# Optimization experiments

Hardware: AMD Instinct MI355X
Metric: run time of the kernel (lower is better)

Reference implementation:

```python
import jax, jax.numpy as jnp
import numpy as np

B, IN, H = 8192, 1024, 1024


def setup_inputs() -> dict:
    key = jax.random.key(0)
    ks = jax.random.split(key, 20)
    std = 1.0 / np.sqrt(H)
    u = lambda k, shape: jax.random.uniform(k, shape, jnp.float32, -std, std)
    inp = {
        "x": jax.random.normal(ks[0], (B, IN), jnp.float32),
        "hx": jax.random.normal(ks[1], (B, H), jnp.float32),
        "cx": jax.random.normal(ks[2], (B, H), jnp.float32),
        "task_id": 0,
        # x2h weights [H, IN] (torch Linear layout) and biases [H]
        "wxi": u(ks[3], (H, IN)), "bxi": u(ks[4], (H,)),
        "wxf": u(ks[5], (H, IN)), "bxf": u(ks[6], (H,)),
        "wxc": u(ks[7], (H, IN)), "bxc": u(ks[8], (H,)),
        "wxo": u(ks[9], (H, IN)), "bxo": u(ks[10], (H,)),
        # h2h weights [H, H] and biases [H]
        "whi": u(ks[11], (H, H)), "bhi": u(ks[12], (H,)),
        "whf": u(ks[13], (H, H)), "bhf": u(ks[14], (H,)),
        "whc": u(ks[15], (H, H)), "bhc": u(ks[16], (H,)),
        "who": u(ks[17], (H, H)), "bho": u(ks[18], (H,)),
    }
    return inp


def reference(x, hx, cx, task_id,
              wxi, bxi, wxf, bxf, wxc, bxc, wxo, bxo,
              whi, bhi, whf, bhf, whc, bhc, who, bho):
    # x = x.view(-1, x.size(1)) is identity for 2D input
    # gate pre-activations: Linear(x) + Linear(hx)  (torch: x @ W.T + b)
    ingate = x @ wxi.T + bxi + hx @ whi.T + bhi
    forgetgate = x @ wxf.T + bxf + hx @ whf.T + bhf
    cellgate = x @ wxc.T + bxc + hx @ whc.T + bhc
    outgate = x @ wxo.T + bxo + hx @ who.T + bho

    i = jax.nn.sigmoid(ingate)
    f = jax.nn.sigmoid(forgetgate)
    g = jnp.tanh(cellgate)
    o = jax.nn.sigmoid(outgate)

    cy = cx * f + i * g
    hy = o * jnp.tanh(cy)
    return hy, cy
```

## Files before the change

kernel.cpp:

```cpp
#include <hip/hip_runtime.h>
#include <hip/hip_bf16.h>

#define B_DIM  8192
#define IN_DIM 1024
#define H_DIM  1024
#define K_DIM  2048

typedef __attribute__((ext_vector_type(8))) short bf16x8;
typedef __attribute__((ext_vector_type(4))) float f32x4;

__device__ __forceinline__ void mfma_16x16x32_bf16(f32x4& d, const bf16x8& a, const bf16x8& b) {
  asm("v_mfma_f32_16x16x32_bf16 %0, %1, %2, %0" : "+v"(d) : "v"(a), "v"(b));
}

__device__ __forceinline__ void gload16(const void* g, void* l) {
  __builtin_amdgcn_global_load_lds(
      (const __attribute__((address_space(1))) void*)g,
      (__attribute__((address_space(3))) void*)l,
      16, 0, 0);
}

__device__ __forceinline__ float fast_sigmoid(float x) {
  return 1.0f / (1.0f + __expf(-x));
}
__device__ __forceinline__ float fast_tanh(float x) {
  float e = __expf(2.0f * x);
  return 1.0f - 2.0f / (e + 1.0f);
}

__global__ __launch_bounds__(256) void pack_a_kernel(
    const float* __restrict__ x, const float* __restrict__ hx,
    __hip_bfloat16* __restrict__ A) {
  const int idx = blockIdx.x * 256 + threadIdx.x;
  const int r  = idx >> 8;
  const int kk = (idx & 255) << 3;
  const float* src = (kk < IN_DIM) ? (x + (size_t)r * IN_DIM + kk)
                                   : (hx + (size_t)r * H_DIM + (kk - IN_DIM));
  const float4 v0 = ((const float4*)src)[0];
  const float4 v1 = ((const float4*)src)[1];
  __hip_bfloat16 t[8];
  t[0] = __float2bfloat16(v0.x); t[1] = __float2bfloat16(v0.y);
  t[2] = __float2bfloat16(v0.z); t[3] = __float2bfloat16(v0.w);
  t[4] = __float2bfloat16(v1.x); t[5] = __float2bfloat16(v1.y);
  t[6] = __float2bfloat16(v1.z); t[7] = __float2bfloat16(v1.w);
  *(uint4*)(A + ((size_t)idx << 3)) = *(const uint4*)t;
}

__global__ __launch_bounds__(256) void pack_w_kernel(
    const float* __restrict__ wxi, const float* __restrict__ wxf,
    const float* __restrict__ wxc, const float* __restrict__ wxo,
    const float* __restrict__ whi, const float* __restrict__ whf,
    const float* __restrict__ whc, const float* __restrict__ who,
    __hip_bfloat16* __restrict__ W) {
  const int idx = blockIdx.x * 256 + threadIdx.x;
  const int row = idx >> 8;
  const int kk  = (idx & 255) << 3;
  const int g = row >> 10, n = row & 1023;
  const float* src;
  if (kk < IN_DIM) {
    const float* p = (g == 0) ? wxi : (g == 1) ? wxf : (g == 2) ? wxc : wxo;
    src = p + (size_t)n * IN_DIM + kk;
  } else {
    const float* p = (g == 0) ? whi : (g == 1) ? whf : (g == 2) ? whc : who;
    src = p + (size_t)n * H_DIM + (kk - IN_DIM);
  }
  const float4 v0 = ((const float4*)src)[0];
  const float4 v1 = ((const float4*)src)[1];
  __hip_bfloat16 t[8];
  t[0] = __float2bfloat16(v0.x); t[1] = __float2bfloat16(v0.y);
  t[2] = __float2bfloat16(v0.z); t[3] = __float2bfloat16(v0.w);
  t[4] = __float2bfloat16(v1.x); t[5] = __float2bfloat16(v1.y);
  t[6] = __float2bfloat16(v1.z); t[7] = __float2bfloat16(v1.w);
  *(uint4*)(W + ((size_t)idx << 3)) = *(const uint4*)t;
}

__global__ __launch_bounds__(256, 2) void lstm_gemm_kernel(
    const __hip_bfloat16* __restrict__ A,
    const __hip_bfloat16* __restrict__ W,
    const float* __restrict__ cx,
    const float* __restrict__ bxi, const float* __restrict__ bhi,
    const float* __restrict__ bxf, const float* __restrict__ bhf,
    const float* __restrict__ bxc, const float* __restrict__ bhc,
    const float* __restrict__ bxo, const float* __restrict__ bho,
    float* __restrict__ hy, float* __restrict__ cy) {

  __shared__ __align__(16) __hip_bfloat16 sA[128][64];
  __shared__ __align__(16) __hip_bfloat16 sW[4][64][64];

  const int tid  = threadIdx.x;
  const int w    = tid >> 6;
  const int lane = tid & 63;
  const int wm = w >> 1, wn = w & 1;
  const int lq = lane >> 4, lr16 = lane & 15;

  const int row0 = blockIdx.x * 128;
  const int col0 = blockIdx.y * 64;

  const int sr  = lane >> 3;
  const int sc  = lane & 7;
  const int scs = sc ^ sr;

  f32x4 acc[4][4][2];
#pragma unroll
  for (int g = 0; g < 4; ++g)
#pragma unroll
    for (int m = 0; m < 4; ++m)
#pragma unroll
      for (int nf = 0; nf < 2; ++nf)
        acc[g][m][nf] = (f32x4){0.f, 0.f, 0.f, 0.f};

  for (int kt = 0; kt < K_DIM / 64; ++kt) {
    const int k0 = kt * 64;
#pragma unroll
    for (int it = 0; it < 4; ++it) {
      const int stripe = it * 4 + w;
      const int fr = stripe * 8 + sr;
      const __hip_bfloat16* src = A + (size_t)(row0 + fr) * K_DIM + k0 + scs * 8;
      gload16(src, (char*)(&sA[0][0]) + stripe * 1024);
    }
#pragma unroll
    for (int it = 0; it < 8; ++it) {
      const int stripe = it * 4 + w;
      const int fr = stripe * 8 + sr;
      const int g = fr >> 6, n = fr & 63;
      const __hip_bfloat16* src =
          W + ((size_t)(g << 10) + col0 + n) * K_DIM + k0 + scs * 8;
      gload16(src, (char*)(&sW[0][0][0]) + stripe * 1024);
    }
    __syncthreads();

#pragma unroll
    for (int ks = 0; ks < 2; ++ks) {
      bf16x8 af[4];
#pragma unroll
      for (int m = 0; m < 4; ++m) {
        const int row = wm * 64 + m * 16 + lr16;
        const int ch  = (ks * 4 + lq) ^ (row & 7);
        af[m] = *(const bf16x8*)&sA[row][ch * 8];
      }
#pragma unroll
      for (int g = 0; g < 4; ++g) {
        bf16x8 bfv[2];
#pragma unroll
        for (int nf = 0; nf < 2; ++nf) {
          const int n  = wn * 32 + nf * 16 + lr16;
          const int ch = (ks * 4 + lq) ^ (n & 7);
          bfv[nf] = *(const bf16x8*)&sW[g][n][ch * 8];
        }
#pragma unroll
        for (int m = 0; m < 4; ++m)
#pragma unroll
          for (int nf = 0; nf < 2; ++nf)
            mfma_16x16x32_bf16(acc[g][m][nf], af[m], bfv[nf]);
      }
    }
    __syncthreads();
  }

#pragma unroll
  for (int nf = 0; nf < 2; ++nf) {
    const int h = col0 + wn * 32 + nf * 16 + lr16;
    const float bi = bxi[h] + bhi[h];
    const float bf = bxf[h] + bhf[h];
    const float bc = bxc[h] + bhc[h];
    const float bo = bxo[h] + bho[h];
#pragma unroll
    for (int m = 0; m < 4; ++m) {
#pragma unroll
      for (int j = 0; j < 4; ++j) {
        const int r = row0 + wm * 64 + m * 16 + lq * 4 + j;
        const size_t o = (size_t)r * H_DIM + h;
        const float ig = fast_sigmoid(acc[0][m][nf][j] + bi);
        const float fg = fast_sigmoid(acc[1][m][nf][j] + bf);
        const float gg = fast_tanh   (acc[2][m][nf][j] + bc);
        const float og = fast_sigmoid(acc[3][m][nf][j] + bo);
        const float c  = cx[o] * fg + ig * gg;
        cy[o] = c;
        hy[o] = og * fast_tanh(c);
      }
    }
  }
}

extern "C" void kernel_launch(void* const* d_in, const int* in_sizes, int n_in,
                              void* d_out, int out_size, void* d_ws, size_t ws_size,
                              hipStream_t stream) {
  const float* x   = (const float*)d_in[0];
  const float* hx  = (const float*)d_in[1];
  const float* cx  = (const float*)d_in[2];
  const float* wxi = (const float*)d_in[4];  const float* bxi = (const float*)d_in[5];
  const float* wxf = (const float*)d_in[6];  const float* bxf = (const float*)d_in[7];
  const float* wxc = (const float*)d_in[8];  const float* bxc = (const float*)d_in[9];
  const float* wxo = (const float*)d_in[10]; const float* bxo = (const float*)d_in[11];
  const float* whi = (const float*)d_in[12]; const float* bhi = (const float*)d_in[13];
  const float* whf = (const float*)d_in[14]; const float* bhf = (const float*)d_in[15];
  const float* whc = (const float*)d_in[16]; const float* bhc = (const float*)d_in[17];
  const float* who = (const float*)d_in[18]; const float* bho = (const float*)d_in[19];

  __hip_bfloat16* Abf = (__hip_bfloat16*)d_ws;
  __hip_bfloat16* Wbf = (__hip_bfloat16*)((char*)d_ws + (size_t)B_DIM * K_DIM * 2);

  float* hy  = (float*)d_out;
  float* cyo = (float*)d_out + (size_t)B_DIM * H_DIM;

  pack_a_kernel<<<(B_DIM * K_DIM / 8) / 256, 256, 0, stream>>>(x, hx, Abf);
  pack_w_kernel<<<(4 * H_DIM * K_DIM / 8) / 256, 256, 0, stream>>>(
      wxi, wxf, wxc, wxo, whi, whf, whc, who, Wbf);

  dim3 grid(B_DIM / 128, H_DIM / 64);
  lstm_gemm_kernel<<<grid, 256, 0, stream>>>(
      Abf, Wbf, cx, bxi, bhi, bxf, bhf, bxc, bhc, bxo, bho, hy, cyo);
}
```

Before: 155.3 us.

## Double-buffer LDS tiles with 256x64 blocks, 8 waves, and phased MFMA/load overlap

Restructures the fused LSTM GEMM so each 512-thread block covers a 256-row by 64-column tile (all four gates), with double-buffered LDS for the A and W tiles. Global-to-LDS loads for the next K step are issued in chunks between MFMA phases, and partial vmcnt waits replace the full syncthreads pairs, so memory latency overlaps compute. It also adds a grouped block-index swizzle for L2 locality and raises MFMA priority with s_setprio. The cost is doubled LDS use (about 128 KB per block) and heavier register pressure, which may limit occupancy.

```diff
diff --git a/kernel.cpp b/kernel.cpp
--- a/kernel.cpp
+++ b/kernel.cpp
@@ -5,6 +5,7 @@
 #define IN_DIM 1024
 #define H_DIM  1024
 #define K_DIM  2048
+#define NT     (K_DIM / 64)
 
 typedef __attribute__((ext_vector_type(8))) short bf16x8;
 typedef __attribute__((ext_vector_type(4))) float f32x4;
@@ -74,7 +75,31 @@
   *(uint4*)(W + ((size_t)idx << 3)) = *(const uint4*)t;
 }
 
-__global__ __launch_bounds__(256, 2) void lstm_gemm_kernel(
+struct PhaseRegs {
+  f32x4 (&acc)[4][8];
+  const bf16x8 (&bfr)[4][2];
+};
+
+template<int MB>
+__device__ __forceinline__ void do_phase(
+    const __hip_bfloat16 (*sAp)[64], f32x4 (&acc)[4][8],
+    const bf16x8 (&bfr)[4][2], int arow, int chk0, int chk1) {
+  bf16x8 a00 = *(const bf16x8*)&sAp[arow + MB * 16][chk0];
+  bf16x8 a01 = *(const bf16x8*)&sAp[arow + MB * 16][chk1];
+  bf16x8 a10 = *(const bf16x8*)&sAp[arow + (MB + 1) * 16][chk0];
+  bf16x8 a11 = *(const bf16x8*)&sAp[arow + (MB + 1) * 16][chk1];
+  __builtin_amdgcn_s_setprio(1);
+#pragma unroll
+  for (int g = 0; g < 4; ++g) {
+    mfma_16x16x32_bf16(acc[g][MB],     a00, bfr[g][0]);
+    mfma_16x16x32_bf16(acc[g][MB],     a01, bfr[g][1]);
+    mfma_16x16x32_bf16(acc[g][MB + 1], a10, bfr[g][0]);
+    mfma_16x16x32_bf16(acc[g][MB + 1], a11, bfr[g][1]);
+  }
+  __builtin_amdgcn_s_setprio(0);
+}
+
+__global__ __launch_bounds__(512, 2) void lstm_gemm_kernel(
     const __hip_bfloat16* __restrict__ A,
     const __hip_bfloat16* __restrict__ W,
     const float* __restrict__ cx,
@@ -84,102 +109,109 @@
     const float* __restrict__ bxo, const float* __restrict__ bho,
     float* __restrict__ hy, float* __restrict__ cy) {
 
-  __shared__ __align__(16) __hip_bfloat16 sA[128][64];
-  __shared__ __align__(16) __hip_bfloat16 sW[4][64][64];
+  __shared__ __align__(16) __hip_bfloat16 sA[2][256][64];
+  __shared__ __align__(16) __hip_bfloat16 sW[2][4][64][64];
 
   const int tid  = threadIdx.x;
   const int w    = tid >> 6;
   const int lane = tid & 63;
-  const int wm = w >> 1, wn = w & 1;
+  const int wm = w >> 2, wn = w & 3;
   const int lq = lane >> 4, lr16 = lane & 15;
 
-  const int row0 = blockIdx.x * 128;
-  const int col0 = blockIdx.y * 64;
-
-  const int sr  = lane >> 3;
-  const int sc  = lane & 7;
-  const int scs = sc ^ sr;
-
-  f32x4 acc[4][4][2];
+  const int bid = blockIdx.x;
+  const int swz = (bid & 7) * 64 + (bid >> 3);
+  const int row0 = (swz >> 4) * 256;
+  const int col0 = (swz & 15) * 64;
+
+  const int srow = tid >> 3;
+  const int scs  = (tid & 7) ^ (srow & 7);
+  const __hip_bfloat16* Asrc = A + (size_t)(row0 + srow) * K_DIM + scs * 8;
+  const __hip_bfloat16* Wsrc = W + (size_t)(col0 + srow) * K_DIM + scs * 8;
+  const size_t Wg = (size_t)H_DIM * K_DIM;
+
+  const int chk0 = ((lq)     ^ (lr16 & 7)) * 8;
+  const int chk1 = ((4 + lq) ^ (lr16 & 7)) * 8;
+  const int arow = wm * 128 + lr16;
+  const int wrow = wn * 16 + lr16;
+
+  f32x4 acc[4][8];
 #pragma unroll
   for (int g = 0; g < 4; ++g)
 #pragma unroll
-    for (int m = 0; m < 4; ++m)
-#pragma unroll
-      for (int nf = 0; nf < 2; ++nf)
-        acc[g][m][nf] = (f32x4){0.f, 0.f, 0.f, 0.f};
-
-  for (int kt = 0; kt < K_DIM / 64; ++kt) {
-    const int k0 = kt * 64;
-#pragma unroll
-    for (int it = 0; it < 4; ++it) {
-      const int stripe = it * 4 + w;
-      const int fr = stripe * 8 + sr;
-      const __hip_bfloat16* src = A + (size_t)(row0 + fr) * K_DIM + k0 + scs * 8;
-      gload16(src, (char*)(&sA[0][0]) + stripe * 1024);
+    for (int m = 0; m < 8; ++m)
+      acc[g][m] = (f32x4){0.f, 0.f, 0.f, 0.f};
+
+#define ISSUE_W2(P, KT, G0)                                                    \
+  {                                                                            \
+    const size_t kof = (size_t)(KT) * 64;                                      \
+    gload16(Wsrc + (size_t)(G0) * Wg + kof,                                    \
+            (char*)&sW[P][G0][0][0] + tid * 16);                               \
+    gload16(Wsrc + (size_t)((G0) + 1) * Wg + kof,                              \
+            (char*)&sW[P][(G0) + 1][0][0] + tid * 16);                         \
+  }
+#define ISSUE_A2(P, KT, R0, R1)                                                \
+  {                                                                            \
+    const size_t kof = (size_t)(KT) * 64;                                      \
+    gload16(Asrc + (size_t)(R0) * K_DIM + kof,                                 \
+            (char*)&sA[P][R0][0] + tid * 16);                                  \
+    gload16(Asrc + (size_t)(R1) * K_DIM + kof,                                 \
+            (char*)&sA[P][R1][0] + tid * 16);                                  \
+  }
+
+  ISSUE_W2(0, 0, 0);
+  ISSUE_W2(0, 0, 2);
+  ISSUE_A2(0, 0, 0, 128);
+  ISSUE_A2(0, 0, 64, 192);
+
+  for (int t = 0; t < NT; ++t) {
+    const int p  = t & 1;
+    const int q  = p ^ 1;
+    const int tn = (t + 1 < NT) ? t + 1 : NT - 1;
+    const __hip_bfloat16(*sAp)[64] = sA[p];
+
+    ISSUE_W2(q, tn, 0);
+    asm volatile("s_waitcnt vmcnt(4)\n\ts_barrier" ::: "memory");
+    bf16x8 bfr[4][2];
+#pragma unroll
+    for (int g = 0; g < 4; ++g) {
+      bfr[g][0] = *(const bf16x8*)&sW[p][g][wrow][chk0];
+      bfr[g][1] = *(const bf16x8*)&sW[p][g][wrow][chk1];
     }
-#pragma unroll
-    for (int it = 0; it < 8; ++it) {
-      const int stripe = it * 4 + w;
-      const int fr = stripe * 8 + sr;
-      const int g = fr >> 6, n = fr & 63;
-      const __hip_bfloat16* src =
-          W + ((size_t)(g << 10) + col0 + n) * K_DIM + k0 + scs * 8;
-      gload16(src, (char*)(&sW[0][0][0]) + stripe * 1024);
+    do_phase<0>(sAp, acc, bfr, arow, chk0, chk1);
+
+    ISSUE_W2(q, tn, 2);
+    do_phase<2>(sAp, acc, bfr, arow, chk0, chk1);
+
+    ISSUE_A2(q, tn, 0, 128);
+    asm volatile("s_waitcnt vmcnt(6)\n\ts_barrier" ::: "memory");
+    do_phase<4>(sAp, acc, bfr, arow, chk0, chk1);
+
+    ISSUE_A2(q, tn, 64, 192);
+    do_phase<6>(sAp, acc, bfr, arow, chk0, chk1);
+  }
+
+  const int h = col0 + wrow;
+  const float bi = bxi[h] + bhi[h];
+  const float bf = bxf[h] + bhf[h];
+  const float bc = bxc[h] + bhc[h];
+  const float bo = bxo[h] + bho[h];
+#pragma unroll
+  for (int m = 0; m < 8; ++m) {
+#pragma unroll
+    for (int j = 0; j < 4; ++j) {
+      const int r = row0 + wm * 128 + m * 16 + lq * 4 + j;
+      const size_t o = (size_t)r * H_DIM + h;
+      const float ig = fast_sigmoid(acc[0][m][j] + bi);
+      const float fg = fast_sigmoid(acc[1][m][j] + bf);
+      const float gg = fast_tanh   (acc[2][m][j] + bc);
+      const float og = fast_sigmoid(acc[3][m][j] + bo);
+      const float c  = cx[o] * fg + ig * gg;
+      cy[o] = c;
+      hy[o] = og * fast_tanh(c);
     }
-    __syncthreads();
-
-#pragma unroll
-    for (int ks = 0; ks < 2; ++ks) {
-      bf16x8 af[4];
-#pragma unroll
-      for (int m = 0; m < 4; ++m) {
-        const int row = wm * 64 + m * 16 + lr16;
-        const int ch  = (ks * 4 + lq) ^ (row & 7);
-        af[m] = *(const bf16x8*)&sA[row][ch * 8];
-      }
-#pragma unroll
-      for (int g = 0; g < 4; ++g) {
-        bf16x8 bfv[2];
-#pragma unroll
-        for (int nf = 0; nf < 2; ++nf) {
-          const int n  = wn * 32 + nf * 16 + lr16;
-          const int ch = (ks * 4 + lq) ^ (n & 7);
-          bfv[nf] = *(const bf16x8*)&sW[g][n][ch * 8];
-        }
-#pragma unroll
-        for (int m = 0; m < 4; ++m)
-#pragma unroll
-          for (int nf = 0; nf < 2; ++nf)
-            mfma_16x16x32_bf16(acc[g][m][nf], af[m], bfv[nf]);
-      }
-    }
-    __syncthreads();
-  }
-
-#pragma unroll
-  for (int nf = 0; nf < 2; ++nf) {
-    const int h = col0 + wn * 32 + nf * 16 + lr16;
-    const float bi = bxi[h] + bhi[h];
-    const float bf = bxf[h] + bhf[h];
-    const float bc = bxc[h] + bhc[h];
-    const float bo = bxo[h] + bho[h];
-#pragma unroll
-    for (int m = 0; m < 4; ++m) {
-#pragma unroll
-      for (int j = 0; j < 4; ++j) {
-        const int r = row0 + wm * 64 + m * 16 + lq * 4 + j;
-        const size_t o = (size_t)r * H_DIM + h;
-        const float ig = fast_sigmoid(acc[0][m][nf][j] + bi);
-        const float fg = fast_sigmoid(acc[1][m][nf][j] + bf);
-        const float gg = fast_tanh   (acc[2][m][nf][j] + bc);
-        const float og = fast_sigmoid(acc[3][m][nf][j] + bo);
-        const float c  = cx[o] * fg + ig * gg;
-        cy[o] = c;
-        hy[o] = og * fast_tanh(c);
-      }
-    }
-  }
+  }
+#undef ISSUE_W2
+#undef ISSUE_A2
 }
 
 extern "C" void kernel_launch(void* const* d_in, const int* in_sizes, int n_in,
@@ -207,7 +239,6 @@
   pack_w_kernel<<<(4 * H_DIM * K_DIM / 8) / 256, 256, 0, stream>>>(
       wxi, wxf, wxc, wxo, whi, whf, whc, who, Wbf);
 
-  dim3 grid(B_DIM / 128, H_DIM / 64);
-  lstm_gemm_kernel<<<grid, 256, 0, stream>>>(
+  lstm_gemm_kernel<<<dim3(512), 512, 0, stream>>>(
       Abf, Wbf, cx, bxi, bhi, bxf, bhf, bxc, bhc, bxo, bho, hy, cyo);
 }
```

Measured after the change: 176.2 us. 13.5% more time.

## Double-buffer LDS with BK=32 prefetch pipeline and swizzled block order

Applied to the files above, without the earlier changes.

The GEMM loop is restructured into a two-stage LDS ping-pong with a K-tile of 32: the next tile's global-to-LDS loads are issued before computing on the current buffer, gated by a partial vmcnt wait plus barrier. The XOR swizzle is dropped in favour of a plain 64-byte row layout, and MFMA sections are wrapped in s_setprio. The grid becomes 1D with a remapped block-to-tile order so neighbouring blocks share weight columns for L2 reuse. The goal is to hide global load latency behind MFMA work. The trade-off is possible LDS bank conflicts from the unswizzled layout and twice as many barriers per unit of K.

```diff
diff --git a/kernel.cpp b/kernel.cpp
--- a/kernel.cpp
+++ b/kernel.cpp
@@ -5,6 +5,8 @@
 #define IN_DIM 1024
 #define H_DIM  1024
 #define K_DIM  2048
+#define BK     32
+#define NT     (K_DIM / BK)
 
 typedef __attribute__((ext_vector_type(8))) short bf16x8;
 typedef __attribute__((ext_vector_type(4))) float f32x4;
@@ -84,8 +86,7 @@
     const float* __restrict__ bxo, const float* __restrict__ bho,
     float* __restrict__ hy, float* __restrict__ cy) {
 
-  __shared__ __align__(16) __hip_bfloat16 sA[128][64];
-  __shared__ __align__(16) __hip_bfloat16 sW[4][64][64];
+  __shared__ __align__(16) char lds[2][24 * 1024];
 
   const int tid  = threadIdx.x;
   const int w    = tid >> 6;
@@ -93,12 +94,37 @@
   const int wm = w >> 1, wn = w & 1;
   const int lq = lane >> 4, lr16 = lane & 15;
 
-  const int row0 = blockIdx.x * 128;
-  const int col0 = blockIdx.y * 64;
-
-  const int sr  = lane >> 3;
-  const int sc  = lane & 7;
-  const int scs = sc ^ sr;
+  const int bid = blockIdx.x;
+  const int row_tile = ((bid & 7) << 3) | ((bid >> 3) & 7);
+  const int col_tile = bid >> 6;
+  const int row0 = row_tile * 128;
+  const int col0 = col_tile * 64;
+
+  const int srow = lane >> 2;
+  const int schk = lane & 3;
+
+  const __hip_bfloat16* gsrc[6];
+  int ldsoff[6];
+#pragma unroll
+  for (int s = 0; s < 6; ++s) {
+    const int seg = w * 6 + s;
+    if (seg < 8) {
+      gsrc[s] = A + (size_t)(row0 + seg * 16 + srow) * K_DIM + schk * 8;
+    } else {
+      const int flat = (seg - 8) * 16 + srow;
+      const int g = flat >> 6, n = flat & 63;
+      gsrc[s] = W + (size_t)((g << 10) + col0 + n) * K_DIM + schk * 8;
+    }
+    ldsoff[s] = seg * 1024;
+  }
+
+#define STAGE(Q, KT)                                                          \
+  {                                                                           \
+    const int koff = (KT) * BK;                                               \
+    _Pragma("unroll")                                                         \
+    for (int s = 0; s < 6; ++s)                                               \
+      gload16(gsrc[s] + koff, &lds[Q][ldsoff[s]]);                            \
+  }
 
   f32x4 acc[4][4][2];
 #pragma unroll
@@ -109,69 +135,59 @@
       for (int nf = 0; nf < 2; ++nf)
         acc[g][m][nf] = (f32x4){0.f, 0.f, 0.f, 0.f};
 
-  for (int kt = 0; kt < K_DIM / 64; ++kt) {
-    const int k0 = kt * 64;
-#pragma unroll
-    for (int it = 0; it < 4; ++it) {
-      const int stripe = it * 4 + w;
-      const int fr = stripe * 8 + sr;
-      const __hip_bfloat16* src = A + (size_t)(row0 + fr) * K_DIM + k0 + scs * 8;
-      gload16(src, (char*)(&sA[0][0]) + stripe * 1024);
-    }
-#pragma unroll
-    for (int it = 0; it < 8; ++it) {
-      const int stripe = it * 4 + w;
-      const int fr = stripe * 8 + sr;
-      const int g = fr >> 6, n = fr & 63;
-      const __hip_bfloat16* src =
-          W + ((size_t)(g << 10) + col0 + n) * K_DIM + k0 + scs * 8;
-      gload16(src, (char*)(&sW[0][0][0]) + stripe * 1024);
-    }
-    __syncthreads();
-
-#pragma unroll
-    for (int ks = 0; ks < 2; ++ks) {
-      bf16x8 af[4];
+  const int aoff = (wm * 64 + lr16) * 64 + lq * 16;
+  const int woff = 8192 + (wn * 32 + lr16) * 64 + lq * 16;
+
+  STAGE(0, 0);
+
+  for (int t = 0; t < NT; ++t) {
+    const int p = t & 1, q = p ^ 1;
+    const int tn = (t + 1 < NT) ? t + 1 : NT - 1;
+
+    STAGE(q, tn);
+    asm volatile("s_waitcnt vmcnt(6)\n\ts_barrier" ::: "memory");
+
+    const char* base = lds[p];
+    bf16x8 af[4];
+#pragma unroll
+    for (int m = 0; m < 4; ++m)
+      af[m] = *(const bf16x8*)(base + aoff + m * (16 * 64));
+
+    __builtin_amdgcn_s_setprio(1);
+#pragma unroll
+    for (int g = 0; g < 4; ++g) {
+      const char* wb = base + woff + g * (64 * 64);
+      const bf16x8 b0 = *(const bf16x8*)(wb);
+      const bf16x8 b1 = *(const bf16x8*)(wb + 16 * 64);
 #pragma unroll
       for (int m = 0; m < 4; ++m) {
-        const int row = wm * 64 + m * 16 + lr16;
-        const int ch  = (ks * 4 + lq) ^ (row & 7);
-        af[m] = *(const bf16x8*)&sA[row][ch * 8];
-      }
-#pragma unroll
-      for (int g = 0; g < 4; ++g) {
-        bf16x8 bfv[2];
-#pragma unroll
-        for (int nf = 0; nf < 2; ++nf) {
-          const int n  = wn * 32 + nf * 16 + lr16;
-          const int ch = (ks * 4 + lq) ^ (n & 7);
-          bfv[nf] = *(const bf16x8*)&sW[g][n][ch * 8];
-        }
-#pragma unroll
-        for (int m = 0; m < 4; ++m)
-#pragma unroll
-          for (int nf = 0; nf < 2; ++nf)
-            mfma_16x16x32_bf16(acc[g][m][nf], af[m], bfv[nf]);
+        mfma_16x16x32_bf16(acc[g][m][0], af[m], b0);
+        mfma_16x16x32_bf16(acc[g][m][1], af[m], b1);
       }
     }
-    __syncthreads();
-  }
-
+    __builtin_amdgcn_s_setprio(0);
+
+    asm volatile("s_barrier" ::: "memory");
+  }
+
+  asm volatile("s_waitcnt vmcnt(0)" ::: "memory");
+
+  const int h = col0 + wn * 32 + lr16;
 #pragma unroll
   for (int nf = 0; nf < 2; ++nf) {
-    const int h = col0 + wn * 32 + nf * 16 + lr16;
-    const float bi = bxi[h] + bhi[h];
-    const float bf = bxf[h] + bhf[h];
-    const float bc = bxc[h] + bhc[h];
-    const float bo = bxo[h] + bho[h];
+    const int hh = h + nf * 16;
+    const float bi = bxi[hh] + bhi[hh];
+    const float bff = bxf[hh] + bhf[hh];
+    const float bc = bxc[hh] + bhc[hh];
+    const float bo = bxo[hh] + bho[hh];
 #pragma unroll
     for (int m = 0; m < 4; ++m) {
 #pragma unroll
       for (int j = 0; j < 4; ++j) {
         const int r = row0 + wm * 64 + m * 16 + lq * 4 + j;
-        const size_t o = (size_t)r * H_DIM + h;
+        const size_t o = (size_t)r * H_DIM + hh;
         const float ig = fast_sigmoid(acc[0][m][nf][j] + bi);
-        const float fg = fast_sigmoid(acc[1][m][nf][j] + bf);
+        const float fg = fast_sigmoid(acc[1][m][nf][j] + bff);
         const float gg = fast_tanh   (acc[2][m][nf][j] + bc);
         const float og = fast_sigmoid(acc[3][m][nf][j] + bo);
         const float c  = cx[o] * fg + ig * gg;
@@ -180,6 +196,7 @@
       }
     }
   }
+#undef STAGE
 }
 
 extern "C" void kernel_launch(void* const* d_in, const int* in_sizes, int n_in,
@@ -207,7 +224,6 @@
   pack_w_kernel<<<(4 * H_DIM * K_DIM / 8) / 256, 256, 0, stream>>>(
       wxi, wxf, wxc, wxo, whi, whf, whc, who, Wbf);
 
-  dim3 grid(B_DIM / 128, H_DIM / 64);
-  lstm_gemm_kernel<<<grid, 256, 0, stream>>>(
+  lstm_gemm_kernel<<<dim3(1024), 256, 0, stream>>>(
       Abf, Wbf, cx, bxi, bhi, bxf, bhf, bxc, bhc, bxo, bho, hy, cyo);
 }
```

Result: slower. 180.6 us (+16.3%).
